# Kernel tuning notes

Hardware: AMD Instinct MI355X
Metric: run time of the kernel (lower is better)

## Reference

```python
import jax, jax.numpy as jnp
import numpy as np
import math

N = 10000; E = 160000; B = 16
H = 256; TD = 128; NB = 4; NL = 3; NAT = 100; CD = 3


def _silu(x):
    return x * jax.nn.sigmoid(x)


def _mlp2(x, w1, b1, w2, b2):
    return _silu(x @ w1 + b1) @ w2 + b2


def _ln(x, g, b):
    m = jnp.mean(x, -1, keepdims=True)
    v = jnp.mean((x - m) ** 2, -1, keepdims=True)
    return (x - m) / jnp.sqrt(v + 1e-5) * g + b


def _fwd(x_atoms, pos, edge_index, batch_idx, timesteps, conditions, emb,
         te_w1, te_b1, te_w2, te_b2, ce_w1, ce_b1, ce_w2, ce_b2,
         tp_w1, tp_b1, tp_w2, tp_b2, nm_w1, nm_b1, nm_w2, nm_b2,
         em_w1, em_b1, em_w2, em_b2, ln_g, ln_b,
         ao_w1, ao_b1, ao_w2, ao_b2, co_w1, co_b1, co_w2, co_b2):
    n = x_atoms.shape[0]
    row, col = edge_index[0], edge_index[1]  # row = source (x_j), col = target (x_i)
    h = emb[x_atoms]  # [N, H]
    half = TD // 2
    freqs = jnp.exp(jnp.arange(half, dtype=jnp.float32) * (-math.log(10000.0) / (half - 1)))
    ang = timesteps.astype(jnp.float32)[:, None] * freqs[None, :]
    time_emb = _mlp2(jnp.concatenate([jnp.sin(ang), jnp.cos(ang)], -1), te_w1, te_b1, te_w2, te_b2)
    time_emb = time_emb + _mlp2(conditions, ce_w1, ce_b1, ce_w2, ce_b2)  # [B, TD]
    rel = pos[row] - pos[col]
    dist = jnp.sqrt(jnp.sum(rel * rel, -1, keepdims=True))  # [E, 1]
    counts = jnp.maximum(
        jax.ops.segment_sum(jnp.ones((row.shape[0],), jnp.float32), col, num_segments=n), 1.0)[:, None]
    for b in range(NB):
        h = h + _mlp2(time_emb, tp_w1[b], tp_b1[b], tp_w2[b], tp_b2[b])[batch_idx]
        for l in range(NL):
            # message: edge_mlp(concat(x_i, x_j, dist)); PyG x_i = target = col, x_j = source = row
            msg = _mlp2(jnp.concatenate([h[col], h[row], dist], -1),
                        em_w1[b, l], em_b1[b, l], em_w2[b, l], em_b2[b, l])  # [E, H]
            agg = jax.ops.segment_sum(msg, col, num_segments=n) / counts  # mean aggregation
            h_new = _mlp2(h, nm_w1[b, l], nm_b1[b, l], nm_w2[b, l], nm_b2[b, l]) + agg
            h = _ln(h + h_new, ln_g[b, l], ln_b[b, l])
    atom = _mlp2(h, ao_w1, ao_b1, ao_w2, ao_b2)  # [N, NAT]
    coord = _mlp2(h, co_w1, co_b1, co_w2, co_b2)  # [N, 3]
    return atom, coord


def setup_inputs() -> dict:
    key = jax.random.key(0)
    ks = jax.random.split(key, 48)
    ki = iter(ks)

    def nrm(shape, s=0.02):
        return jax.random.normal(next(ki), shape, jnp.float32) * s

    x_atoms = jax.random.randint(next(ki), (N,), 0, NAT)
    pos = jax.random.normal(next(ki), (N, 3), jnp.float32)
    row = jax.random.randint(next(ki), (E,), 0, N)
    off = jax.random.randint(next(ki), (E,), 1, N)
    col = (row + off) % N  # avoid self-loops so dist > 0
    edge_index = jnp.stack([row, col])
    batch_idx = jnp.sort(jax.random.randint(next(ki), (N,), 0, B))
    timesteps = jax.random.randint(next(ki), (B,), 0, 1000)
    conditions = jax.random.normal(next(ki), (B, CD), jnp.float32)
    z = lambda s: jnp.zeros(s, jnp.float32)
    params = dict(
        emb=nrm((NAT, H)),
        te_w1=nrm((TD, 2 * TD)), te_b1=z((2 * TD,)), te_w2=nrm((2 * TD, TD)), te_b2=z((TD,)),
        ce_w1=nrm((CD, H)), ce_b1=z((H,)), ce_w2=nrm((H, TD)), ce_b2=z((TD,)),
        tp_w1=nrm((NB, TD, H)), tp_b1=z((NB, H)), tp_w2=nrm((NB, H, H)), tp_b2=z((NB, H)),
        nm_w1=nrm((NB, NL, H, H)), nm_b1=z((NB, NL, H)), nm_w2=nrm((NB, NL, H, H)), nm_b2=z((NB, NL, H)),
        em_w1=nrm((NB, NL, 2 * H + 1, H)), em_b1=z((NB, NL, H)), em_w2=nrm((NB, NL, H, H)), em_b2=z((NB, NL, H)),
        ln_g=jnp.ones((NB, NL, H), jnp.float32), ln_b=z((NB, NL, H)),
        ao_w1=nrm((H, H)), ao_b1=z((H,)), ao_w2=nrm((H, NAT)), ao_b2=z((NAT,)),
        co_w1=nrm((H, H)), co_b1=z((H,)), co_w2=nrm((H, 3)), co_b2=z((3,)),
    )
    return dict(x_atoms=x_atoms, pos=pos, edge_index=edge_index, batch_idx=batch_idx,
                timesteps=timesteps, conditions=conditions, **params)


def reference(x_atoms, pos, edge_index, batch_idx, timesteps, conditions, emb,
              te_w1, te_b1, te_w2, te_b2, ce_w1, ce_b1, ce_w2, ce_b2,
              tp_w1, tp_b1, tp_w2, tp_b2, nm_w1, nm_b1, nm_w2, nm_b2,
              em_w1, em_b1, em_w2, em_b2, ln_g, ln_b,
              ao_w1, ao_b1, ao_w2, ao_b2, co_w1, co_b1, co_w2, co_b2):
    return _fwd(x_atoms, pos, edge_index, batch_idx, timesteps, conditions, emb,
                te_w1, te_b1, te_w2, te_b2, ce_w1, ce_b1, ce_w2, ce_b2,
                tp_w1, tp_b1, tp_w2, tp_b2, nm_w1, nm_b1, nm_w2, nm_b2,
                em_w1, em_b1, em_w2, em_b2, ln_g, ln_b,
                ao_w1, ao_b1, ao_w2, ao_b2, co_w1, co_b1, co_w2, co_b2)
```

## Files before the change

kernel.cpp:

```cpp
#include <hip/hip_runtime.h>

typedef unsigned short u16;
typedef __attribute__((ext_vector_type(8))) short   bf16x8;
typedef __attribute__((ext_vector_type(4))) float   f32x4;
typedef __attribute__((ext_vector_type(4))) unsigned short u16x4;
typedef __attribute__((ext_vector_type(2))) unsigned short u16x2;

#define DEV __device__ __forceinline__

DEV float bf2f(u16 u){ return __uint_as_float(((unsigned)u)<<16); }
DEV u16 f2bf(float f){ unsigned x=__float_as_uint(f); unsigned r=x+0x7fffu+((x>>16)&1u); return (u16)(r>>16); }
DEV float silu_f(float x){
  float e = __expf(-x);
  return x * __builtin_amdgcn_rcpf(1.f + e);
}
DEV float ldf(const void* p, long i, int isbf){
  float r;
  if (isbf) r = bf2f(((const u16*)p)[i]);
  else      r = ((const float*)p)[i];
  return r;
}
template<int ISBF> DEV float LD(const void* p, long i){
  if (ISBF) return bf2f(((const u16*)p)[i]);
  return ((const float*)p)[i];
}

#define GLDS(g,l) __builtin_amdgcn_global_load_lds((const __attribute__((address_space(1))) void*)(g), (__attribute__((address_space(3))) void*)(l), 16, 0, 0)

DEV int xcd_swz(int bid, int nwg){
  int q = nwg >> 3, r = nwg & 7;
  int x = bid & 7, l = bid >> 3;
  return (x < r ? x*(q+1) : r*(q+1) + (x-r)*q) + l;
}

__global__ __launch_bounds__(256) void k_packparams(
    const void* nm_b1, const void* em_b1, const void* nm_b2, const void* em_b2,
    const void* ln_g, const void* ln_b, const void* em_w1,
    const void* ao_b1, const void* co_b1, const void* ao_b2,
    const void* co_w2, const void* co_b2,
    int* __restrict__ flagp, float* __restrict__ pp){
  int isbf = (((const unsigned*)ln_g)[0] == 0x3F800000u) ? 0 : 1;
  int i = blockIdx.x*256 + threadIdx.x;
  if (i == 0) flagp[0] = isbf;
  if (i >= 22887) return;
  const int T1 = 3072;
  float v;
  if      (i < T1)    v = ldf(nm_b1, i, isbf);
  else if (i < 2*T1)  v = ldf(em_b1, i-T1, isbf);
  else if (i < 3*T1)  v = ldf(nm_b2, i-2*T1, isbf);
  else if (i < 4*T1)  v = ldf(em_b2, i-3*T1, isbf);
  else if (i < 5*T1)  v = ldf(ln_g, i-4*T1, isbf);
  else if (i < 6*T1)  v = ldf(ln_b, i-5*T1, isbf);
  else if (i < 7*T1){ int j=i-6*T1; int li=j>>8; v = ldf(em_w1, (long)li*513*256 + 512*256 + (j&255), isbf); }
  else if (i < 22016){ int j=i-21504; v = (j<256) ? ldf(ao_b1,j,isbf) : ldf(co_b1,j-256,isbf); }
  else if (i < 22116) v = ldf(ao_b2, i-22016, isbf);
  else if (i < 22884) v = ldf(co_w2, i-22116, isbf);
  else                v = ldf(co_b2, i-22884, isbf);
  pp[i] = v;
}

struct WTJob {
  const void* in; long inoff; long ims; long obase; long oms;
  u16* out; int istride; int Ncin; int ors; int gx; int gy;
};
struct WTJobs { WTJob j[8]; int tile0[8]; };

template<int ISBF>
DEV void wtall_body(const WTJobs& J){
  int bidx = blockIdx.x;
  int ji = 0;
  #pragma unroll
  for (int j=1;j<8;j++) if (bidx >= J.tile0[j]) ji = j;
  const WTJob& job = J.j[ji];
  int ti = bidx - J.tile0[ji];
  int kx = ti % job.gx;
  int jy = (ti / job.gx) % job.gy;
  long m  = ti / (job.gx * job.gy);
  int k0 = kx*64, j0 = jy*64;
  __shared__ float tile[64][65];
  int t = threadIdx.x;
  int c = t & 63, r4 = t >> 6;
  #pragma unroll
  for (int pass=0; pass<16; pass++){
    int k = k0 + pass*4 + r4;
    int j = j0 + c;
    float v = 0.f;
    if (j < job.Ncin) v = LD<ISBF>(job.in, job.inoff + m*job.ims + (long)k*job.istride + j);
    tile[pass*4 + r4][c] = v;
  }
  __syncthreads();
  #pragma unroll
  for (int pass=0; pass<16; pass++){
    int j = j0 + pass*4 + r4;
    int k = k0 + c;
    job.out[m*job.oms + job.obase + (long)j*job.ors + k] = f2bf(tile[c][pass*4 + r4]);
  }
}
__global__ __launch_bounds__(256) void k_wtall(WTJobs J, const int* __restrict__ flagp){
  if (flagp[0]) wtall_body<1>(J);
  else          wtall_body<0>(J);
}

template<int ISBF>
DEV void time_body(const int* tsteps, const void* cond,
    const void* te_w1, const void* te_b1, const void* te_w2, const void* te_b2,
    const void* ce_w1, const void* ce_b1, const void* ce_w2, const void* ce_b2,
    const void* tp_w1, const void* tp_b1, const void* tp_w2, const void* tp_b2,
    float* tpe){
  __shared__ float wbuf[8192];
  __shared__ float sa[256], sb[256], tm[256], tb[128];
  int b4 = blockIdx.x >> 4, b = blockIdx.x & 15, t = threadIdx.x;
  float ts = (float)tsteps[b];
  if (t < 64){
    float coef = (float)(-9.210340371976184/63.0);
    float fr = __expf(coef * (float)t);
    float ang = ts * fr;
    sa[t]      = sinf(ang);
    sa[64 + t] = cosf(ang);
  }
  __syncthreads();
  float a1 = LD<ISBF>(te_b1, t);
  for (int ck=0; ck<128; ck+=32){
    for (int i=t;i<8192;i+=256) wbuf[i] = LD<ISBF>(te_w1, (long)ck*256 + i);
    __syncthreads();
    #pragma unroll 8
    for (int k=0;k<32;k++) a1 += sa[ck+k]*wbuf[k*256+t];
    __syncthreads();
  }
  sb[t] = silu_f(a1);
  float te = (t<128) ? LD<ISBF>(te_b2, t) : 0.f;
  for (int ck=0; ck<256; ck+=64){
    for (int i=t;i<8192;i+=256) wbuf[i] = LD<ISBF>(te_w2, (long)ck*128 + i);
    __syncthreads();
    if (t<128){
      #pragma unroll 8
      for (int k=0;k<64;k++) te += sb[ck+k]*wbuf[k*128+t];
    }
    __syncthreads();
  }
  float a2 = LD<ISBF>(ce_b1, t);
  #pragma unroll
  for (int k=0;k<3;k++) a2 += LD<ISBF>(cond, b*3+k)*LD<ISBF>(ce_w1, k*256+t);
  sa[t] = silu_f(a2);
  float ce = (t<128) ? LD<ISBF>(ce_b2, t) : 0.f;
  for (int ck=0; ck<256; ck+=64){
    for (int i=t;i<8192;i+=256) wbuf[i] = LD<ISBF>(ce_w2, (long)ck*128 + i);
    __syncthreads();
    if (t<128){
      #pragma unroll 8
      for (int k=0;k<64;k++) ce += sa[ck+k]*wbuf[k*128+t];
    }
    __syncthreads();
  }
  if (t<128) tb[t] = te + ce;
  float a3 = LD<ISBF>(tp_b1, b4*256 + t);
  for (int ck=0; ck<128; ck+=32){
    for (int i=t;i<8192;i+=256) wbuf[i] = LD<ISBF>(tp_w1, ((long)b4*128+ck)*256 + i);
    __syncthreads();
    #pragma unroll 8
    for (int k=0;k<32;k++) a3 += tb[ck+k]*wbuf[k*256+t];
    __syncthreads();
  }
  tm[t] = silu_f(a3);
  float a4 = LD<ISBF>(tp_b2, b4*256 + t);
  for (int ck=0; ck<256; ck+=32){
    for (int i=t;i<8192;i+=256) wbuf[i] = LD<ISBF>(tp_w2, ((long)b4*256+ck)*256 + i);
    __syncthreads();
    #pragma unroll 8
    for (int k=0;k<32;k++) a4 += tm[ck+k]*wbuf[k*256+t];
    __syncthreads();
  }
  tpe[((long)b4*16 + b)*256 + t] = a4;
}
__global__ __launch_bounds__(256) void k_time(
    const int* tsteps, const void* cond,
    const void* te_w1, const void* te_b1, const void* te_w2, const void* te_b2,
    const void* ce_w1, const void* ce_b1, const void* ce_w2, const void* ce_b2,
    const void* tp_w1, const void* tp_b1, const void* tp_w2, const void* tp_b2,
    const int* __restrict__ flagp, float* tpe){
  if (flagp[0]) time_body<1>(tsteps,cond,te_w1,te_b1,te_w2,te_b2,ce_w1,ce_b1,ce_w2,ce_b2,tp_w1,tp_b1,tp_w2,tp_b2,tpe);
  else          time_body<0>(tsteps,cond,te_w1,te_b1,te_w2,te_b2,ce_w1,ce_b1,ce_w2,ce_b2,tp_w1,tp_b1,tp_w2,tp_b2,tpe);
}

template<int ISBF>
DEV void edgegeo_body(const int* ei, const void* pos, float* dist, int* cnt, int E){
  int e = blockIdx.x*256 + threadIdx.x;
  if (e >= E) return;
  int r = ei[e], c = ei[E + e];
  float dx = LD<ISBF>(pos,(long)r*3+0) - LD<ISBF>(pos,(long)c*3+0);
  float dy = LD<ISBF>(pos,(long)r*3+1) - LD<ISBF>(pos,(long)c*3+1);
  float dz = LD<ISBF>(pos,(long)r*3+2) - LD<ISBF>(pos,(long)c*3+2);
  dist[e] = sqrtf(dx*dx + dy*dy + dz*dz);
  atomicAdd(&cnt[c], 1);
}
__global__ __launch_bounds__(256) void k_edgegeo(const int* ei, const void* pos,
                          const int* __restrict__ flagp, float* dist, int* cnt, int E){
  if (flagp[0]) edgegeo_body<1>(ei,pos,dist,cnt,E);
  else          edgegeo_body<0>(ei,pos,dist,cnt,E);
}

__global__ __launch_bounds__(1024) void k_scan(const int* __restrict__ cnt, int* __restrict__ basep, int n){
  __shared__ int wsum[16];
  int t = threadIdx.x, w = t >> 6, lane = t & 63;
  int running = 0;
  int nch = (n + 1023) >> 10;
  for (int ch=0; ch<nch; ch++){
    int i = ch*1024 + t;
    int v = (i < n) ? cnt[i] : 0;
    int sc = v;
    #pragma unroll
    for (int off=1; off<64; off<<=1){
      int u = __shfl_up(sc, off, 64);
      if (lane >= off) sc += u;
    }
    if (lane == 63) wsum[w] = sc;
    __syncthreads();
    int wexcl = 0, tot = 0;
    #pragma unroll
    for (int j=0;j<16;j++){ int x = wsum[j]; if (j < w) wexcl += x; tot += x; }
    if (i < n) basep[i] = running + wexcl + sc - v;
    running += tot;
    __syncthreads();
  }
  if (t == 0) basep[n] = running;
}

__global__ __launch_bounds__(256) void k_scatter(const int* __restrict__ ei, const int* __restrict__ basep,
                          int* __restrict__ cursor, int* __restrict__ perm, int E){
  int e = blockIdx.x*256 + threadIdx.x;
  if (e >= E) return;
  int c = ei[E + e];
  int p = atomicAdd(&cursor[c], 1);
  perm[basep[c] + p] = e;
}

template<int ISBF>
DEV void embed_body(const int* xa, const void* emb, const float* tpe0, const int* bidx,
                    float* h, u16* hb, int total){
  int idx = blockIdx.x*256 + threadIdx.x;
  if (idx >= total) return;
  int row = idx >> 8, col = idx & 255;
  float v = LD<ISBF>(emb, (long)xa[row]*256 + col) + tpe0[bidx[row]*256 + col];
  h[idx] = v;
  hb[idx] = f2bf(v);
}
__global__ __launch_bounds__(256) void k_embed(const int* xa, const void* emb,
                        const int* __restrict__ flagp, const float* tpe0, const int* bidx,
                        float* h, u16* hb, int total){
  if (flagp[0]) embed_body<1>(xa, emb, tpe0, bidx, h, hb, total);
  else          embed_body<0>(xa, emb, tpe0, bidx, h, hb, total);
}

__global__ __launch_bounds__(256) void k_agg(
    const u16* __restrict__ PQ, const int* __restrict__ perm, const int* __restrict__ basep,
    const int* __restrict__ rows, const float* __restrict__ dist,
    const float* __restrict__ w1rf, const float* __restrict__ b1f,
    const int* __restrict__ cnt, u16* __restrict__ A2, int n){
  int w = threadIdx.x >> 6, lane = threadIdx.x & 63;
  int node = blockIdx.x*2 + (w >> 1);
  if (node >= n) return;
  int half = w & 1;
  int c0 = half*128 + lane*2;
  u16x2 pv = *(const u16x2*)&PQ[(long)node*512 + c0];
  float pb0 = bf2f(pv[0]) + b1f[c0];
  float pb1 = bf2f(pv[1]) + b1f[c0+1];
  float wr0 = w1rf[c0], wr1 = w1rf[c0+1];
  float acc0 = 0.f, acc1 = 0.f;
  int s = basep[node], e = basep[node+1];
  const u16* Qb = PQ + 256 + c0;
  for (int q0=s; q0<e; q0+=64){
    int m = e - q0; if (m > 64) m = 64;
    int   rl = 0; float dl = 0.f;
    if (lane < m){ int ed = perm[q0+lane]; rl = rows[ed]; dl = dist[ed]; }
    int q = 0;
    for (; q+4<=m; q+=4){
      int   r0 = __shfl(rl, q,   64), r1 = __shfl(rl, q+1, 64);
      int   r2 = __shfl(rl, q+2, 64), r3 = __shfl(rl, q+3, 64);
      float d0 = __shfl(dl, q,   64), d1 = __shfl(dl, q+1, 64);
      float d2 = __shfl(dl, q+2, 64), d3 = __shfl(dl, q+3, 64);
      u16x2 qv0 = *(const u16x2*)&Qb[(long)r0*512];
      u16x2 qv1 = *(const u16x2*)&Qb[(long)r1*512];
      u16x2 qv2 = *(const u16x2*)&Qb[(long)r2*512];
      u16x2 qv3 = *(const u16x2*)&Qb[(long)r3*512];
      acc0 += silu_f(fmaf(d0, wr0, pb0 + bf2f(qv0[0])));
      acc1 += silu_f(fmaf(d0, wr1, pb1 + bf2f(qv0[1])));
      acc0 += silu_f(fmaf(d1, wr0, pb0 + bf2f(qv1[0])));
      acc1 += silu_f(fmaf(d1, wr1, pb1 + bf2f(qv1[1])));
      acc0 += silu_f(fmaf(d2, wr0, pb0 + bf2f(qv2[0])));
      acc1 += silu_f(fmaf(d2, wr1, pb1 + bf2f(qv2[1])));
      acc0 += silu_f(fmaf(d3, wr0, pb0 + bf2f(qv3[0])));
      acc1 += silu_f(fmaf(d3, wr1, pb1 + bf2f(qv3[1])));
    }
    for (; q<m; q++){
      int   r = __shfl(rl, q, 64);
      float d = __shfl(dl, q, 64);
      u16x2 qv = *(const u16x2*)&Qb[(long)r*512];
      acc0 += silu_f(fmaf(d, wr0, pb0 + bf2f(qv[0])));
      acc1 += silu_f(fmaf(d, wr1, pb1 + bf2f(qv[1])));
    }
  }
  int cc = cnt[node];
  float inv = __builtin_amdgcn_rcpf((float)(cc > 0 ? cc : 1));
  u16x2 o; o[0] = f2bf(acc0*inv); o[1] = f2bf(acc1*inv);
  *(u16x2*)&A2[(long)node*512 + 256 + c0] = o;
}

__global__ __launch_bounds__(256) void k_co2(
    const u16* __restrict__ UV, const float* __restrict__ w, const float* __restrict__ b,
    const int* __restrict__ flagp, void* __restrict__ out, long n100, int n){
  int isbf = flagp[0];
  int row = blockIdx.x*4 + (threadIdx.x >> 6);
  if (row >= n) return;
  int lane = threadIdx.x & 63;
  int k0 = lane*4;
  u16x4 vv = *(const u16x4*)&UV[(long)row*512 + 256 + k0];
  float a0=0.f, a1=0.f, a2=0.f;
  #pragma unroll
  for (int j=0;j<4;j++){
    float v = bf2f(vv[j]);
    a0 += v*w[(k0+j)*3+0];
    a1 += v*w[(k0+j)*3+1];
    a2 += v*w[(k0+j)*3+2];
  }
  #pragma unroll
  for (int o=32;o>=1;o>>=1){ a0 += __shfl_xor(a0,o,64); a1 += __shfl_xor(a1,o,64); a2 += __shfl_xor(a2,o,64); }
  if (lane == 0){
    float r0 = a0 + b[0], r1 = a1 + b[1], r2 = a2 + b[2];
    if (isbf){
      u16* o = (u16*)out + n100 + (long)row*3;
      o[0] = f2bf(r0); o[1] = f2bf(r1); o[2] = f2bf(r2);
    } else {
      float* o = (float*)out + n100 + (long)row*3;
      o[0] = r0; o[1] = r1; o[2] = r2;
    }
  }
}

template<int TM, int MODE>
__global__ __launch_bounds__(256) void k_gemm(
    const u16* __restrict__ A, int lda, const u16* __restrict__ Wt,
    void* __restrict__ D0, void* __restrict__ D1,
    const float* __restrict__ bf1,
    const int* __restrict__ flagp, int M, int K, int nbn){
  constexpr int MR = TM/32;
  __shared__ __align__(16) u16 As[TM*64];
  __shared__ __align__(16) u16 Bs[128*64];
  const int bid = xcd_swz(blockIdx.x, gridDim.x);
  const int mb = bid / nbn, nb = bid - mb*nbn;
  const int bm0 = mb*TM, bn0 = nb*128;
  const int t = threadIdx.x;
  const int w = t >> 6, lane = t & 63;
  const int wr = w >> 1, wc = w & 1;
  const int swz8 = ((lane & 7) ^ (lane >> 3)) * 8;

  f32x4 acc[MR][4];
  #pragma unroll
  for (int m=0;m<MR;m++)
    #pragma unroll
    for (int n=0;n<4;n++){ f32x4 z = {0.f,0.f,0.f,0.f}; acc[m][n] = z; }

  long baseA[TM/32];
  #pragma unroll
  for (int i=0;i<TM/32;i++){
    int r = bm0 + i*32 + w*8 + (lane>>3);
    if (r > M-1) r = M-1;
    baseA[i] = (long)r*lda + swz8;
  }
  long baseB[4];
  #pragma unroll
  for (int i=0;i<4;i++){
    int r = bn0 + i*32 + w*8 + (lane>>3);
    baseB[i] = (long)r*K + swz8;
  }

  const int rA = lane & 15;
  const int sx = rA & 7;
  const int qhi = lane >> 4;

  for (int kt=0; kt<K; kt+=64){
    #pragma unroll
    for (int i=0;i<TM/32;i++) GLDS(A  + baseA[i] + kt, As + (i*32 + w*8)*64);
    #pragma unroll
    for (int i=0;i<4;i++)     GLDS(Wt + baseB[i] + kt, Bs + (i*32 + w*8)*64);
    __syncthreads();
    #pragma unroll
    for (int kk=0;kk<2;kk++){
      const int punit = ((kk*4 + qhi) ^ sx) * 8;
      bf16x8 af[MR], bv[4];
      #pragma unroll
      for (int m=0;m<MR;m++)
        af[m] = *(const bf16x8*)&As[(wr*(TM/2) + m*16 + rA)*64 + punit];
      #pragma unroll
      for (int n=0;n<4;n++)
        bv[n] = *(const bf16x8*)&Bs[(wc*64 + n*16 + rA)*64 + punit];
      #pragma unroll
      for (int m=0;m<MR;m++)
        #pragma unroll
        for (int n=0;n<4;n++)
          acc[m][n] = __builtin_amdgcn_mfma_f32_16x16x32_bf16(af[m], bv[n], acc[m][n], 0, 0, 0);
    }
    __syncthreads();
  }

  const int rg = lane >> 4, cix = lane & 15;
  const int isbf = (MODE==3) ? flagp[0] : 0;
  #pragma unroll
  for (int n=0;n<4;n++){
    const int col = bn0 + wc*64 + n*16 + cix;
    float b1v = 0.f;
    if (MODE==0){ if (col>=512) b1v = bf1[col-512]; }
    else if (MODE==2){ b1v = bf1[col]; }
    else { if (col<100) b1v = bf1[col]; }
    #pragma unroll
    for (int m=0;m<MR;m++){
      const int rbase = bm0 + wr*(TM/2) + m*16 + rg*4;
      #pragma unroll
      for (int r=0;r<4;r++){
        const int row = rbase + r;
        if (row >= M) continue;
        float v = acc[m][n][r];
        if (MODE==0){
          if (col < 512) ((u16*)D0)[(long)row*512 + col] = f2bf(v);
          else           ((u16*)D1)[(long)row*512 + (col-512)] = f2bf(silu_f(v + b1v));
        } else if (MODE==2){
          ((u16*)D0)[(long)row*512 + col] = f2bf(silu_f(v + b1v));
        } else {
          if (col < 100){
            v += b1v;
            if (isbf) ((u16*)D0)[(long)row*100 + col] = f2bf(v);
            else      ((float*)D0)[(long)row*100 + col] = v;
          }
        }
      }
    }
  }
}

__global__ __launch_bounds__(256) void k_gemmln(
    const u16* __restrict__ A, const u16* __restrict__ Wt,
    float* __restrict__ h, u16* __restrict__ hb,
    const float* __restrict__ b1f, const float* __restrict__ b2f,
    const float* __restrict__ gf, const float* __restrict__ bbf,
    const int* __restrict__ cnt,
    const float* __restrict__ tpe, const int* __restrict__ bidx,
    int M, int K){
  __shared__ __align__(16) u16 As[32*64];
  __shared__ __align__(16) u16 Bs[256*64];
  const int bm0 = blockIdx.x*32;
  const int t = threadIdx.x;
  const int w = t >> 6, lane = t & 63;
  const int wc = w;
  const int swz8 = ((lane & 7) ^ (lane >> 3)) * 8;

  f32x4 acc[2][4];
  #pragma unroll
  for (int m=0;m<2;m++)
    #pragma unroll
    for (int n=0;n<4;n++){ f32x4 z = {0.f,0.f,0.f,0.f}; acc[m][n] = z; }

  long baseA;
  { int r = bm0 + w*8 + (lane>>3); if (r > M-1) r = M-1; baseA = (long)r*512 + swz8; }
  long baseB[8];
  #pragma unroll
  for (int i=0;i<8;i++){
    int r = i*32 + w*8 + (lane>>3);
    baseB[i] = (long)r*K + swz8;
  }

  const int rA = lane & 15;
  const int sx = rA & 7;
  const int qhi = lane >> 4;

  for (int kt=0; kt<K; kt+=64){
    GLDS(A + baseA + kt, As + (w*8)*64);
    #pragma unroll
    for (int i=0;i<8;i++) GLDS(Wt + baseB[i] + kt, Bs + (i*32 + w*8)*64);
    __syncthreads();
    #pragma unroll
    for (int kk=0;kk<2;kk++){
      const int punit = ((kk*4 + qhi) ^ sx) * 8;
      bf16x8 af[2], bv[4];
      #pragma unroll
      for (int m=0;m<2;m++)
        af[m] = *(const bf16x8*)&As[(m*16 + rA)*64 + punit];
      #pragma unroll
      for (int n=0;n<4;n++)
        bv[n] = *(const bf16x8*)&Bs[(wc*64 + n*16 + rA)*64 + punit];
      #pragma unroll
      for (int m=0;m<2;m++)
        #pragma unroll
        for (int n=0;n<4;n++)
          acc[m][n] = __builtin_amdgcn_mfma_f32_16x16x32_bf16(af[m], bv[n], acc[m][n], 0, 0, 0);
    }
    __syncthreads();
  }

  const int rg = lane >> 4, cix = lane & 15;
  float ps[2][4], pq[2][4];
  #pragma unroll
  for (int m=0;m<2;m++){
    #pragma unroll
    for (int r=0;r<4;r++){
      const int row = bm0 + m*16 + rg*4 + r;
      const int rowc = (row < M) ? row : (M-1);
      const float hmask = (cnt[rowc] > 0) ? 1.f : 0.f;
      float s = 0.f, q = 0.f;
      #pragma unroll
      for (int n=0;n<4;n++){
        const int col = wc*64 + n*16 + cix;
        float v = acc[m][n][r] + b1f[col] + hmask*b2f[col] + h[(long)rowc*256 + col];
        acc[m][n][r] = v;
        s += v; q += v*v;
      }
      ps[m][r] = s; pq[m][r] = q;
    }
  }
  #pragma unroll
  for (int m=0;m<2;m++)
    #pragma unroll
    for (int r=0;r<4;r++){
      #pragma unroll
      for (int o=8;o>=1;o>>=1){
        ps[m][r] += __shfl_xor(ps[m][r], o, 64);
        pq[m][r] += __shfl_xor(pq[m][r], o, 64);
      }
    }
  float* sred = (float*)As;
  if (cix == 0){
    #pragma unroll
    for (int m=0;m<2;m++)
      #pragma unroll
      for (int r=0;r<4;r++){
        int rl = m*16 + rg*4 + r;
        sred[w*32 + rl]       = ps[m][r];
        sred[128 + w*32 + rl] = pq[m][r];
      }
  }
  __syncthreads();
  #pragma unroll
  for (int m=0;m<2;m++){
    #pragma unroll
    for (int r=0;r<4;r++){
      const int rl = m*16 + rg*4 + r;
      const int row = bm0 + rl;
      if (row >= M) continue;
      float S = sred[rl] + sred[32+rl] + sred[64+rl] + sred[96+rl];
      float Q = sred[128+rl] + sred[160+rl] + sred[192+rl] + sred[224+rl];
      float mean = S * (1.f/256.f);
      float var  = Q * (1.f/256.f) - mean*mean;
      float rs = rsqrtf(var + 1e-5f);
      const float* tb = tpe ? (tpe + (long)bidx[row]*256) : nullptr;
      #pragma unroll
      for (int n=0;n<4;n++){
        const int col = wc*64 + n*16 + cix;
        float y = (acc[m][n][r]-mean)*rs*gf[col] + bbf[col];
        if (tb) y += tb[col];
        h[(long)row*256 + col] = y;
        hb[(long)row*256 + col] = f2bf(y);
      }
    }
  }
}

extern "C" void kernel_launch(void* const* d_in, const int* in_sizes, int n_in,
                              void* d_out, int out_size, void* d_ws, size_t ws_size,
                              hipStream_t stream)
{
  const int N  = in_sizes[0];
  const int E  = in_sizes[2] / 2;
  const int H  = 256;
  const int MB128 = (N + 127)/128;
  const int MB64  = (N + 63)/64;
  const int MB32  = (N + 31)/32;

  const int*  x_atoms = (const int*)d_in[0];
  const void* pos     = d_in[1];
  const int*  ei      = (const int*)d_in[2];
  const int*  bidx    = (const int*)d_in[3];
  const int*  tsteps  = (const int*)d_in[4];
  const void* cond    = d_in[5];
  const void* emb     = d_in[6];
  const void* te_w1   = d_in[7];
  const void* te_b1   = d_in[8];
  const void* te_w2   = d_in[9];
  const void* te_b2   = d_in[10];
  const void* ce_w1   = d_in[11];
  const void* ce_b1   = d_in[12];
  const void* ce_w2   = d_in[13];
  const void* ce_b2   = d_in[14];
  const void* tp_w1   = d_in[15];
  const void* tp_b1   = d_in[16];
  const void* tp_w2   = d_in[17];
  const void* tp_b2   = d_in[18];
  const void* nm_w1   = d_in[19];
  const void* nm_b1   = d_in[20];
  const void* nm_w2   = d_in[21];
  const void* nm_b2   = d_in[22];
  const void* em_w1   = d_in[23];
  const void* em_b1   = d_in[24];
  const void* em_w2   = d_in[25];
  const void* em_b2   = d_in[26];
  const void* ln_g    = d_in[27];
  const void* ln_b    = d_in[28];
  const void* ao_w1   = d_in[29];
  const void* ao_b1   = d_in[30];
  const void* ao_w2   = d_in[31];
  const void* ao_b2   = d_in[32];
  const void* co_w1   = d_in[33];
  const void* co_b1   = d_in[34];
  const void* co_w2   = d_in[35];
  const void* co_b2   = d_in[36];

  char* wp = (char*)d_ws;
  auto alloc = [&](size_t bytes)->char*{ char* p = wp; wp += (bytes + 255) & ~(size_t)255; return p; };
  int*   flagp   = (int*)  alloc(256);
  float* h_f32   = (float*)alloc((size_t)N*H*4);
  u16*   hb16    = (u16*)  alloc((size_t)N*H*2);
  u16*   PQ      = (u16*)  alloc((size_t)N*512*2);
  u16*   A2      = (u16*)  alloc((size_t)N*512*2);
  u16*   UV      = PQ;
  float* dist    = (float*)alloc((size_t)E*4);
  int*   perm    = (int*)  alloc((size_t)E*4);
  int*   basep   = (int*)  alloc((size_t)(N+1)*4);
  int*   cnt     = (int*)  alloc((size_t)N*4);
  int*   cursor  = (int*)  alloc((size_t)N*4);
  float* tpe     = (float*)alloc((size_t)4*16*256*4);
  u16*   pqtW    = (u16*)  alloc((size_t)12*768*256*2);
  u16*   w2stk   = (u16*)  alloc((size_t)12*256*512*2);
  u16*   UVw     = (u16*)  alloc((size_t)512*256*2);
  u16*   ao_w2t  = (u16*)  alloc((size_t)128*256*2);
  float* pp      = (float*)alloc((size_t)22887*4);

  const float* nm_b1f = pp;
  const float* em_b1f = pp + 3072;
  const float* nm_b2f = pp + 6144;
  const float* em_b2f = pp + 9216;
  const float* ln_gf  = pp + 12288;
  const float* ln_bf  = pp + 15360;
  const float* w1rf   = pp + 18432;
  const float* headbf = pp + 21504;
  const float* ao_b2f = pp + 22016;
  const float* co_w2f = pp + 22116;
  const float* co_b2f = pp + 22884;

  hipMemsetAsync(cnt,    0, (size_t)N*4, stream);
  hipMemsetAsync(cursor, 0, (size_t)N*4, stream);

  k_packparams<<<(22887+255)/256, 256, 0, stream>>>(nm_b1, em_b1, nm_b2, em_b2, ln_g, ln_b, em_w1,
                                                    ao_b1, co_b1, ao_b2, co_w2, co_b2, flagp, pp);

  WTJobs J;
  auto setjob = [&](int idx, const void* in, long inoff, long ims, int istride, int Ncin,
                    u16* out, long obase, int ors, long oms, int gx, int gy, int gz){
    J.j[idx] = WTJob{ in, inoff, ims, obase, oms, out, istride, Ncin, ors, gx, gy };
    J.tile0[idx] = (idx == 0) ? 0 : 0;
    return gx*gy*gz;
  };
  int tacc = 0;
  int tn;
  tn = setjob(0, em_w1, 0,        513*256, 256, 256, pqtW,  0,        256, 768*256, 4, 4, 12); J.tile0[0]=tacc; tacc+=tn;
  tn = setjob(1, em_w1, 256*256,  513*256, 256, 256, pqtW,  256*256,  256, 768*256, 4, 4, 12); J.tile0[1]=tacc; tacc+=tn;
  tn = setjob(2, nm_w1, 0,        256*256, 256, 256, pqtW,  512*256,  256, 768*256, 4, 4, 12); J.tile0[2]=tacc; tacc+=tn;
  tn = setjob(3, nm_w2, 0,        256*256, 256, 256, w2stk, 0,        512, 256*512, 4, 4, 12); J.tile0[3]=tacc; tacc+=tn;
  tn = setjob(4, em_w2, 0,        256*256, 256, 256, w2stk, 256,      512, 256*512, 4, 4, 12); J.tile0[4]=tacc; tacc+=tn;
  tn = setjob(5, ao_w1, 0,        0,       256, 256, UVw,   0,        256, 0,       4, 4, 1);  J.tile0[5]=tacc; tacc+=tn;
  tn = setjob(6, co_w1, 0,        0,       256, 256, UVw,   256*256,  256, 0,       4, 4, 1);  J.tile0[6]=tacc; tacc+=tn;
  tn = setjob(7, ao_w2, 0,        0,       100, 100, ao_w2t,0,        256, 0,       4, 2, 1);  J.tile0[7]=tacc; tacc+=tn;
  k_wtall<<<tacc, 256, 0, stream>>>(J, flagp);

  k_time<<<64, 256, 0, stream>>>(tsteps, cond, te_w1, te_b1, te_w2, te_b2,
                                 ce_w1, ce_b1, ce_w2, ce_b2,
                                 tp_w1, tp_b1, tp_w2, tp_b2, flagp, tpe);

  k_edgegeo<<<(E+255)/256, 256, 0, stream>>>(ei, pos, flagp, dist, cnt, E);
  k_scan<<<1, 1024, 0, stream>>>(cnt, basep, N);
  k_scatter<<<(E+255)/256, 256, 0, stream>>>(ei, basep, cursor, perm, E);

  k_embed<<<(N*H+255)/256, 256, 0, stream>>>(x_atoms, emb, flagp, tpe, bidx, h_f32, hb16, N*H);

  for (int b4 = 0; b4 < 4; b4++){
    for (int l = 0; l < 3; l++){
      int li = b4*3 + l;
      k_gemm<128,0><<<MB128*6, 256, 0, stream>>>(hb16, 256, pqtW + (long)li*768*256,
                                                 PQ, A2, nm_b1f + li*256,
                                                 flagp, N, 256, 6);
      k_agg<<<(N+1)/2, 256, 0, stream>>>(PQ, perm, basep, ei, dist,
                                         w1rf + li*256, em_b1f + li*256, cnt, A2, N);
      const float* tpe_next = (l == 2 && b4 < 3) ? (tpe + (long)(b4+1)*16*256) : nullptr;
      k_gemmln<<<MB32, 256, 0, stream>>>(A2, w2stk + (long)li*256*512,
                                         h_f32, hb16,
                                         nm_b2f + li*256, em_b2f + li*256,
                                         ln_gf + li*256, ln_bf + li*256,
                                         cnt, tpe_next, bidx, N, 512);
    }
  }

  k_gemm<128,2><<<MB128*4, 256, 0, stream>>>(hb16, 256, UVw, UV, nullptr, headbf,
                                             flagp, N, 256, 4);
  k_gemm<64,3><<<MB64*1, 256, 0, stream>>>(UV, 512, ao_w2t, d_out, nullptr, ao_b2f,
                                           flagp, N, 256, 1);
  k_co2<<<(N+3)/4, 256, 0, stream>>>(UV, co_w2f, co_b2f, flagp, d_out, (long)N*100, N);
}
```

Measured before the change: 875.2 us.

## Fuse startup kernels and merge edge aggregation into LayerNorm GEMM

Four preprocessing launches (time MLP, weight transposes, param packing, edge geometry) are merged into one k_startup kernel, with the f32 time path double-buffered through global_load_lds. Scatter and embed are fused into one launch, and the dtype flag is now taken from ln_g inside each kernel instead of from a device flag. Per-layer k_agg and k_gemmln are merged into k_aggln, which aggregates edges into LDS and feeds that directly into the second GEMM. This drops the A2 intermediate buffer and several launches, but the fused kernel does more work per block and runs on fewer blocks (MB32).

```diff
diff --git a/kernel.cpp b/kernel.cpp
--- a/kernel.cpp
+++ b/kernel.cpp
@@ -24,6 +24,9 @@
   if (ISBF) return bf2f(((const u16*)p)[i]);
   return ((const float*)p)[i];
 }
+DEV int detect_bf(const void* lng){
+  return (((const unsigned*)lng)[0] == 0x3F800000u) ? 0 : 1;
+}
 
 #define GLDS(g,l) __builtin_amdgcn_global_load_lds((const __attribute__((address_space(1))) void*)(g), (__attribute__((address_space(3))) void*)(l), 16, 0, 0)
 
@@ -33,15 +36,48 @@
   return (x < r ? x*(q+1) : r*(q+1) + (x-r)*q) + l;
 }
 
-__global__ __launch_bounds__(256) void k_packparams(
+struct WTJob {
+  const void* in; u16* out;
+  int inoff, ims, obase, oms, istride, Ncin, ors, gx, gy;
+};
+struct WTJobs { WTJob j[8]; int tile0[8]; };
+
+template<int ISBF>
+DEV void wtall_body(const WTJobs& J, int bidx, float* tile ){
+  int ji = 0;
+  #pragma unroll
+  for (int j=1;j<8;j++) if (bidx >= J.tile0[j]) ji = j;
+  const WTJob& job = J.j[ji];
+  int ti = bidx - J.tile0[ji];
+  int kx = ti % job.gx;
+  int jy = (ti / job.gx) % job.gy;
+  long m  = ti / (job.gx * job.gy);
+  int k0 = kx*64, j0 = jy*64;
+  int t = threadIdx.x;
+  int c = t & 63, r4 = t >> 6;
+  #pragma unroll
+  for (int pass=0; pass<16; pass++){
+    int k = k0 + pass*4 + r4;
+    int j = j0 + c;
+    float v = 0.f;
+    if (j < job.Ncin) v = LD<ISBF>(job.in, (long)job.inoff + m*job.ims + (long)k*job.istride + j);
+    tile[(pass*4 + r4)*65 + c] = v;
+  }
+  __syncthreads();
+  #pragma unroll
+  for (int pass=0; pass<16; pass++){
+    int j = j0 + pass*4 + r4;
+    int k = k0 + c;
+    job.out[m*job.oms + job.obase + (long)j*job.ors + k] = f2bf(tile[c*65 + pass*4 + r4]);
+  }
+}
+
+DEV void pack_body(int pb, int isbf,
     const void* nm_b1, const void* em_b1, const void* nm_b2, const void* em_b2,
     const void* ln_g, const void* ln_b, const void* em_w1,
     const void* ao_b1, const void* co_b1, const void* ao_b2,
-    const void* co_w2, const void* co_b2,
-    int* __restrict__ flagp, float* __restrict__ pp){
-  int isbf = (((const unsigned*)ln_g)[0] == 0x3F800000u) ? 0 : 1;
-  int i = blockIdx.x*256 + threadIdx.x;
-  if (i == 0) flagp[0] = isbf;
+    const void* co_w2, const void* co_b2, float* pp){
+  int i = pb*256 + threadIdx.x;
   if (i >= 22887) return;
   const int T1 = 3072;
   float v;
@@ -59,132 +95,9 @@
   pp[i] = v;
 }
 
-struct WTJob {
-  const void* in; long inoff; long ims; long obase; long oms;
-  u16* out; int istride; int Ncin; int ors; int gx; int gy;
-};
-struct WTJobs { WTJob j[8]; int tile0[8]; };
-
 template<int ISBF>
-DEV void wtall_body(const WTJobs& J){
-  int bidx = blockIdx.x;
-  int ji = 0;
-  #pragma unroll
-  for (int j=1;j<8;j++) if (bidx >= J.tile0[j]) ji = j;
-  const WTJob& job = J.j[ji];
-  int ti = bidx - J.tile0[ji];
-  int kx = ti % job.gx;
-  int jy = (ti / job.gx) % job.gy;
-  long m  = ti / (job.gx * job.gy);
-  int k0 = kx*64, j0 = jy*64;
-  __shared__ float tile[64][65];
-  int t = threadIdx.x;
-  int c = t & 63, r4 = t >> 6;
-  #pragma unroll
-  for (int pass=0; pass<16; pass++){
-    int k = k0 + pass*4 + r4;
-    int j = j0 + c;
-    float v = 0.f;
-    if (j < job.Ncin) v = LD<ISBF>(job.in, job.inoff + m*job.ims + (long)k*job.istride + j);
-    tile[pass*4 + r4][c] = v;
-  }
-  __syncthreads();
-  #pragma unroll
-  for (int pass=0; pass<16; pass++){
-    int j = j0 + pass*4 + r4;
-    int k = k0 + c;
-    job.out[m*job.oms + job.obase + (long)j*job.ors + k] = f2bf(tile[c][pass*4 + r4]);
-  }
-}
-__global__ __launch_bounds__(256) void k_wtall(WTJobs J, const int* __restrict__ flagp){
-  if (flagp[0]) wtall_body<1>(J);
-  else          wtall_body<0>(J);
-}
-
-template<int ISBF>
-DEV void time_body(const int* tsteps, const void* cond,
-    const void* te_w1, const void* te_b1, const void* te_w2, const void* te_b2,
-    const void* ce_w1, const void* ce_b1, const void* ce_w2, const void* ce_b2,
-    const void* tp_w1, const void* tp_b1, const void* tp_w2, const void* tp_b2,
-    float* tpe){
-  __shared__ float wbuf[8192];
-  __shared__ float sa[256], sb[256], tm[256], tb[128];
-  int b4 = blockIdx.x >> 4, b = blockIdx.x & 15, t = threadIdx.x;
-  float ts = (float)tsteps[b];
-  if (t < 64){
-    float coef = (float)(-9.210340371976184/63.0);
-    float fr = __expf(coef * (float)t);
-    float ang = ts * fr;
-    sa[t]      = sinf(ang);
-    sa[64 + t] = cosf(ang);
-  }
-  __syncthreads();
-  float a1 = LD<ISBF>(te_b1, t);
-  for (int ck=0; ck<128; ck+=32){
-    for (int i=t;i<8192;i+=256) wbuf[i] = LD<ISBF>(te_w1, (long)ck*256 + i);
-    __syncthreads();
-    #pragma unroll 8
-    for (int k=0;k<32;k++) a1 += sa[ck+k]*wbuf[k*256+t];
-    __syncthreads();
-  }
-  sb[t] = silu_f(a1);
-  float te = (t<128) ? LD<ISBF>(te_b2, t) : 0.f;
-  for (int ck=0; ck<256; ck+=64){
-    for (int i=t;i<8192;i+=256) wbuf[i] = LD<ISBF>(te_w2, (long)ck*128 + i);
-    __syncthreads();
-    if (t<128){
-      #pragma unroll 8
-      for (int k=0;k<64;k++) te += sb[ck+k]*wbuf[k*128+t];
-    }
-    __syncthreads();
-  }
-  float a2 = LD<ISBF>(ce_b1, t);
-  #pragma unroll
-  for (int k=0;k<3;k++) a2 += LD<ISBF>(cond, b*3+k)*LD<ISBF>(ce_w1, k*256+t);
-  sa[t] = silu_f(a2);
-  float ce = (t<128) ? LD<ISBF>(ce_b2, t) : 0.f;
-  for (int ck=0; ck<256; ck+=64){
-    for (int i=t;i<8192;i+=256) wbuf[i] = LD<ISBF>(ce_w2, (long)ck*128 + i);
-    __syncthreads();
-    if (t<128){
-      #pragma unroll 8
-      for (int k=0;k<64;k++) ce += sa[ck+k]*wbuf[k*128+t];
-    }
-    __syncthreads();
-  }
-  if (t<128) tb[t] = te + ce;
-  float a3 = LD<ISBF>(tp_b1, b4*256 + t);
-  for (int ck=0; ck<128; ck+=32){
-    for (int i=t;i<8192;i+=256) wbuf[i] = LD<ISBF>(tp_w1, ((long)b4*128+ck)*256 + i);
-    __syncthreads();
-    #pragma unroll 8
-    for (int k=0;k<32;k++) a3 += tb[ck+k]*wbuf[k*256+t];
-    __syncthreads();
-  }
-  tm[t] = silu_f(a3);
-  float a4 = LD<ISBF>(tp_b2, b4*256 + t);
-  for (int ck=0; ck<256; ck+=32){
-    for (int i=t;i<8192;i+=256) wbuf[i] = LD<ISBF>(tp_w2, ((long)b4*256+ck)*256 + i);
-    __syncthreads();
-    #pragma unroll 8
-    for (int k=0;k<32;k++) a4 += tm[ck+k]*wbuf[k*256+t];
-    __syncthreads();
-  }
-  tpe[((long)b4*16 + b)*256 + t] = a4;
-}
-__global__ __launch_bounds__(256) void k_time(
-    const int* tsteps, const void* cond,
-    const void* te_w1, const void* te_b1, const void* te_w2, const void* te_b2,
-    const void* ce_w1, const void* ce_b1, const void* ce_w2, const void* ce_b2,
-    const void* tp_w1, const void* tp_b1, const void* tp_w2, const void* tp_b2,
-    const int* __restrict__ flagp, float* tpe){
-  if (flagp[0]) time_body<1>(tsteps,cond,te_w1,te_b1,te_w2,te_b2,ce_w1,ce_b1,ce_w2,ce_b2,tp_w1,tp_b1,tp_w2,tp_b2,tpe);
-  else          time_body<0>(tsteps,cond,te_w1,te_b1,te_w2,te_b2,ce_w1,ce_b1,ce_w2,ce_b2,tp_w1,tp_b1,tp_w2,tp_b2,tpe);
-}
-
-template<int ISBF>
-DEV void edgegeo_body(const int* ei, const void* pos, float* dist, int* cnt, int E){
-  int e = blockIdx.x*256 + threadIdx.x;
+DEV void edgegeo_body(int eb, const int* ei, const void* pos, float* dist, int* cnt, int E){
+  int e = eb*256 + threadIdx.x;
   if (e >= E) return;
   int r = ei[e], c = ei[E + e];
   float dx = LD<ISBF>(pos,(long)r*3+0) - LD<ISBF>(pos,(long)c*3+0);
@@ -193,10 +106,185 @@
   dist[e] = sqrtf(dx*dx + dy*dy + dz*dz);
   atomicAdd(&cnt[c], 1);
 }
-__global__ __launch_bounds__(256) void k_edgegeo(const int* ei, const void* pos,
-                          const int* __restrict__ flagp, float* dist, int* cnt, int E){
-  if (flagp[0]) edgegeo_body<1>(ei,pos,dist,cnt,E);
-  else          edgegeo_body<0>(ei,pos,dist,cnt,E);
+
+DEV void time_body_f32(const int* tsteps, const float* cond,
+    const float* te_w1,const float* te_b1,const float* te_w2,const float* te_b2,
+    const float* ce_w1,const float* ce_b1,const float* ce_w2,const float* ce_b2,
+    const float* tp_w1,const float* tp_b1,const float* tp_w2,const float* tp_b2,
+    float* tpe, float* smem){
+  float* wbuf = smem;
+  float* sa = smem + 16384;
+  float* sb = sa + 256;
+  float* tm = sb + 256;
+  float* tb = tm + 256;
+  const int b4 = blockIdx.x >> 4, b = blockIdx.x & 15, t = threadIdx.x;
+  const int wbase = (t >> 6) * 256;
+
+  auto TISSUE = [&](const float* src, int buf){
+    float* d = wbuf + buf*8192 + wbase;
+    #pragma unroll
+    for (int r=0;r<8;r++)
+      GLDS(src + (long)r*1024 + t*4, d + r*1024);
+  };
+
+  float ts = (float)tsteps[b];
+  if (t < 64){
+    float coef = (float)(-9.210340371976184/63.0);
+    float fr = __expf(coef * (float)t);
+    float ang = ts * fr;
+    sa[t] = sinf(ang); sa[64+t] = cosf(ang);
+  }
+  TISSUE(te_w1, 0);
+  __syncthreads();
+  float a1 = te_b1[t];
+  for (int c=0;c<4;c++){
+    if (c<3) TISSUE(te_w1 + (c+1)*8192, (c+1)&1);
+    const float* wb = wbuf + (c&1)*8192;
+    #pragma unroll 8
+    for (int k=0;k<32;k++) a1 = fmaf(sa[c*32+k], wb[k*256+t], a1);
+    __syncthreads();
+  }
+  sb[t] = silu_f(a1);
+  TISSUE(te_w2, 0);
+  __syncthreads();
+  float te = (t<128) ? te_b2[t] : 0.f;
+  for (int c=0;c<4;c++){
+    if (c<3) TISSUE(te_w2 + (c+1)*8192, (c+1)&1);
+    const float* wb = wbuf + (c&1)*8192;
+    if (t < 128){
+      #pragma unroll 8
+      for (int k=0;k<64;k++) te = fmaf(sb[c*64+k], wb[k*128+t], te);
+    }
+    __syncthreads();
+  }
+  {
+    float a2 = ce_b1[t];
+    #pragma unroll
+    for (int k=0;k<3;k++) a2 = fmaf(cond[b*3+k], ce_w1[k*256+t], a2);
+    sa[t] = silu_f(a2);
+  }
+  TISSUE(ce_w2, 0);
+  __syncthreads();
+  float ce = (t<128) ? ce_b2[t] : 0.f;
+  for (int c=0;c<4;c++){
+    if (c<3) TISSUE(ce_w2 + (c+1)*8192, (c+1)&1);
+    const float* wb = wbuf + (c&1)*8192;
+    if (t < 128){
+      #pragma unroll 8
+      for (int k=0;k<64;k++) ce = fmaf(sa[c*64+k], wb[k*128+t], ce);
+    }
+    __syncthreads();
+  }
+  if (t < 128) tb[t] = te + ce;
+  const float* W5 = tp_w1 + (long)b4*128*256;
+  TISSUE(W5, 0);
+  __syncthreads();
+  float a3 = tp_b1[b4*256 + t];
+  for (int c=0;c<4;c++){
+    if (c<3) TISSUE(W5 + (c+1)*8192, (c+1)&1);
+    const float* wb = wbuf + (c&1)*8192;
+    #pragma unroll 8
+    for (int k=0;k<32;k++) a3 = fmaf(tb[c*32+k], wb[k*256+t], a3);
+    __syncthreads();
+  }
+  tm[t] = silu_f(a3);
+  const float* W6 = tp_w2 + (long)b4*256*256;
+  TISSUE(W6, 0);
+  __syncthreads();
+  float a4 = tp_b2[b4*256 + t];
+  for (int c=0;c<8;c++){
+    if (c<7) TISSUE(W6 + (c+1)*8192, (c+1)&1);
+    const float* wb = wbuf + (c&1)*8192;
+    #pragma unroll 8
+    for (int k=0;k<32;k++) a4 = fmaf(tm[c*32+k], wb[k*256+t], a4);
+    __syncthreads();
+  }
+  tpe[((long)b4*16 + b)*256 + t] = a4;
+}
+
+DEV void time_body_bf16(const int* tsteps, const u16* cond,
+    const u16* te_w1,const u16* te_b1,const u16* te_w2,const u16* te_b2,
+    const u16* ce_w1,const u16* ce_b1,const u16* ce_w2,const u16* ce_b2,
+    const u16* tp_w1,const u16* tp_b1,const u16* tp_w2,const u16* tp_b2,
+    float* tpe, float* smem){
+  float* sa = smem; float* sb = smem+256; float* tm = smem+512; float* tb = smem+768;
+  int b4 = blockIdx.x >> 4, b = blockIdx.x & 15, t = threadIdx.x;
+  float ts = (float)tsteps[b];
+  if (t < 64){
+    float coef = (float)(-9.210340371976184/63.0);
+    float fr = __expf(coef * (float)t);
+    float ang = ts * fr;
+    sa[t] = sinf(ang); sa[64+t] = cosf(ang);
+  }
+  __syncthreads();
+  float a1 = bf2f(te_b1[t]);
+  for (int k=0;k<128;k++) a1 += sa[k]*bf2f(te_w1[k*256+t]);
+  __syncthreads();
+  sb[t] = silu_f(a1);
+  __syncthreads();
+  float te = 0.f;
+  if (t<128){
+    te = bf2f(te_b2[t]);
+    for (int k=0;k<256;k++) te += sb[k]*bf2f(te_w2[k*128+t]);
+  }
+  float a2 = bf2f(ce_b1[t]);
+  for (int k=0;k<3;k++) a2 += bf2f(cond[b*3+k])*bf2f(ce_w1[k*256+t]);
+  float t2v = silu_f(a2);
+  __syncthreads();
+  sa[t] = t2v;
+  __syncthreads();
+  if (t<128){
+    float ce = bf2f(ce_b2[t]);
+    for (int k=0;k<256;k++) ce += sa[k]*bf2f(ce_w2[k*128+t]);
+    tb[t] = te + ce;
+  }
+  __syncthreads();
+  float a3 = bf2f(tp_b1[b4*256+t]);
+  for (int k=0;k<128;k++) a3 += tb[k]*bf2f(tp_w1[((long)b4*128+k)*256+t]);
+  __syncthreads();
+  tm[t] = silu_f(a3);
+  __syncthreads();
+  float a4 = bf2f(tp_b2[b4*256+t]);
+  for (int k=0;k<256;k++) a4 += tm[k]*bf2f(tp_w2[((long)b4*256+k)*256+t]);
+  tpe[((long)b4*16+b)*256+t] = a4;
+}
+
+__global__ __launch_bounds__(256) void k_startup(
+    const int* tsteps, const void* cond,
+    const void* te_w1,const void* te_b1,const void* te_w2,const void* te_b2,
+    const void* ce_w1,const void* ce_b1,const void* ce_w2,const void* ce_b2,
+    const void* tp_w1,const void* tp_b1,const void* tp_w2,const void* tp_b2,
+    float* tpe,
+    WTJobs J, int wt_n,
+    const void* nm_b1,const void* em_b1,const void* nm_b2,const void* em_b2,
+    const void* ln_g,const void* ln_b,const void* em_w1,
+    const void* ao_b1,const void* co_b1,const void* ao_b2,const void* co_w2,const void* co_b2,
+    float* pp, int pack_n,
+    const int* ei, const void* pos, float* dist, int* cnt, int E)
+{
+  __shared__ __align__(16) float smem[17408];
+  const int isbf = detect_bf(ln_g);
+  int b = blockIdx.x;
+  if (b < 64){
+    if (isbf) time_body_bf16(tsteps, (const u16*)cond,
+        (const u16*)te_w1,(const u16*)te_b1,(const u16*)te_w2,(const u16*)te_b2,
+        (const u16*)ce_w1,(const u16*)ce_b1,(const u16*)ce_w2,(const u16*)ce_b2,
+        (const u16*)tp_w1,(const u16*)tp_b1,(const u16*)tp_w2,(const u16*)tp_b2, tpe, smem);
+    else time_body_f32(tsteps, (const float*)cond,
+        (const float*)te_w1,(const float*)te_b1,(const float*)te_w2,(const float*)te_b2,
+        (const float*)ce_w1,(const float*)ce_b1,(const float*)ce_w2,(const float*)ce_b2,
+        (const float*)tp_w1,(const float*)tp_b1,(const float*)tp_w2,(const float*)tp_b2, tpe, smem);
+  } else if (b < 64 + wt_n){
+    if (isbf) wtall_body<1>(J, b-64, smem);
+    else      wtall_body<0>(J, b-64, smem);
+  } else if (b < 64 + wt_n + pack_n){
+    pack_body(b - 64 - wt_n, isbf, nm_b1, em_b1, nm_b2, em_b2, ln_g, ln_b, em_w1,
+              ao_b1, co_b1, ao_b2, co_w2, co_b2, pp);
+  } else {
+    int eb = b - 64 - wt_n - pack_n;
+    if (isbf) edgegeo_body<1>(eb, ei, pos, dist, cnt, E);
+    else      edgegeo_body<0>(eb, ei, pos, dist, cnt, E);
+  }
 }
 
 __global__ __launch_bounds__(1024) void k_scan(const int* __restrict__ cnt, int* __restrict__ basep, int n){
@@ -225,90 +313,35 @@
   if (t == 0) basep[n] = running;
 }
 
-__global__ __launch_bounds__(256) void k_scatter(const int* __restrict__ ei, const int* __restrict__ basep,
-                          int* __restrict__ cursor, int* __restrict__ perm, int E){
-  int e = blockIdx.x*256 + threadIdx.x;
-  if (e >= E) return;
-  int c = ei[E + e];
-  int p = atomicAdd(&cursor[c], 1);
-  perm[basep[c] + p] = e;
-}
-
-template<int ISBF>
-DEV void embed_body(const int* xa, const void* emb, const float* tpe0, const int* bidx,
-                    float* h, u16* hb, int total){
-  int idx = blockIdx.x*256 + threadIdx.x;
-  if (idx >= total) return;
-  int row = idx >> 8, col = idx & 255;
-  float v = LD<ISBF>(emb, (long)xa[row]*256 + col) + tpe0[bidx[row]*256 + col];
-  h[idx] = v;
-  hb[idx] = f2bf(v);
-}
-__global__ __launch_bounds__(256) void k_embed(const int* xa, const void* emb,
-                        const int* __restrict__ flagp, const float* tpe0, const int* bidx,
-                        float* h, u16* hb, int total){
-  if (flagp[0]) embed_body<1>(xa, emb, tpe0, bidx, h, hb, total);
-  else          embed_body<0>(xa, emb, tpe0, bidx, h, hb, total);
-}
-
-__global__ __launch_bounds__(256) void k_agg(
-    const u16* __restrict__ PQ, const int* __restrict__ perm, const int* __restrict__ basep,
-    const int* __restrict__ rows, const float* __restrict__ dist,
-    const float* __restrict__ w1rf, const float* __restrict__ b1f,
-    const int* __restrict__ cnt, u16* __restrict__ A2, int n){
-  int w = threadIdx.x >> 6, lane = threadIdx.x & 63;
-  int node = blockIdx.x*2 + (w >> 1);
-  if (node >= n) return;
-  int half = w & 1;
-  int c0 = half*128 + lane*2;
-  u16x2 pv = *(const u16x2*)&PQ[(long)node*512 + c0];
-  float pb0 = bf2f(pv[0]) + b1f[c0];
-  float pb1 = bf2f(pv[1]) + b1f[c0+1];
-  float wr0 = w1rf[c0], wr1 = w1rf[c0+1];
-  float acc0 = 0.f, acc1 = 0.f;
-  int s = basep[node], e = basep[node+1];
-  const u16* Qb = PQ + 256 + c0;
-  for (int q0=s; q0<e; q0+=64){
-    int m = e - q0; if (m > 64) m = 64;
-    int   rl = 0; float dl = 0.f;
-    if (lane < m){ int ed = perm[q0+lane]; rl = rows[ed]; dl = dist[ed]; }
-    int q = 0;
-    for (; q+4<=m; q+=4){
-      int   r0 = __shfl(rl, q,   64), r1 = __shfl(rl, q+1, 64);
-      int   r2 = __shfl(rl, q+2, 64), r3 = __shfl(rl, q+3, 64);
-      float d0 = __shfl(dl, q,   64), d1 = __shfl(dl, q+1, 64);
-      float d2 = __shfl(dl, q+2, 64), d3 = __shfl(dl, q+3, 64);
-      u16x2 qv0 = *(const u16x2*)&Qb[(long)r0*512];
-      u16x2 qv1 = *(const u16x2*)&Qb[(long)r1*512];
-      u16x2 qv2 = *(const u16x2*)&Qb[(long)r2*512];
-      u16x2 qv3 = *(const u16x2*)&Qb[(long)r3*512];
-      acc0 += silu_f(fmaf(d0, wr0, pb0 + bf2f(qv0[0])));
-      acc1 += silu_f(fmaf(d0, wr1, pb1 + bf2f(qv0[1])));
-      acc0 += silu_f(fmaf(d1, wr0, pb0 + bf2f(qv1[0])));
-      acc1 += silu_f(fmaf(d1, wr1, pb1 + bf2f(qv1[1])));
-      acc0 += silu_f(fmaf(d2, wr0, pb0 + bf2f(qv2[0])));
-      acc1 += silu_f(fmaf(d2, wr1, pb1 + bf2f(qv2[1])));
-      acc0 += silu_f(fmaf(d3, wr0, pb0 + bf2f(qv3[0])));
-      acc1 += silu_f(fmaf(d3, wr1, pb1 + bf2f(qv3[1])));
-    }
-    for (; q<m; q++){
-      int   r = __shfl(rl, q, 64);
-      float d = __shfl(dl, q, 64);
-      u16x2 qv = *(const u16x2*)&Qb[(long)r*512];
-      acc0 += silu_f(fmaf(d, wr0, pb0 + bf2f(qv[0])));
-      acc1 += silu_f(fmaf(d, wr1, pb1 + bf2f(qv[1])));
-    }
-  }
-  int cc = cnt[node];
-  float inv = __builtin_amdgcn_rcpf((float)(cc > 0 ? cc : 1));
-  u16x2 o; o[0] = f2bf(acc0*inv); o[1] = f2bf(acc1*inv);
-  *(u16x2*)&A2[(long)node*512 + 256 + c0] = o;
+__global__ __launch_bounds__(256) void k_scatter_embed(
+    const int* __restrict__ ei, const int* __restrict__ basep,
+    int* __restrict__ cursor, int* __restrict__ perm, int E,
+    const int* __restrict__ xa, const void* __restrict__ emb, const void* __restrict__ lng,
+    const float* __restrict__ tpe0, const int* __restrict__ bidx,
+    float* __restrict__ h, u16* __restrict__ hb, int totalh){
+  int b = blockIdx.x, t = threadIdx.x;
+  int nsb = (E + 255) >> 8;
+  if (b < nsb){
+    int e = b*256 + t;
+    if (e >= E) return;
+    int c = ei[E + e];
+    int p = atomicAdd(&cursor[c], 1);
+    perm[basep[c] + p] = e;
+  } else {
+    int isbf = detect_bf(lng);
+    int idx = (b - nsb)*256 + t;
+    if (idx >= totalh) return;
+    int row = idx >> 8, col = idx & 255;
+    float v = ldf(emb, (long)xa[row]*256 + col, isbf) + tpe0[bidx[row]*256 + col];
+    h[idx] = v;
+    hb[idx] = f2bf(v);
+  }
 }
 
 __global__ __launch_bounds__(256) void k_co2(
     const u16* __restrict__ UV, const float* __restrict__ w, const float* __restrict__ b,
-    const int* __restrict__ flagp, void* __restrict__ out, long n100, int n){
-  int isbf = flagp[0];
+    const void* __restrict__ lng, void* __restrict__ out, long n100, int n){
+  int isbf = detect_bf(lng);
   int row = blockIdx.x*4 + (threadIdx.x >> 6);
   if (row >= n) return;
   int lane = threadIdx.x & 63;
@@ -341,7 +374,7 @@
     const u16* __restrict__ A, int lda, const u16* __restrict__ Wt,
     void* __restrict__ D0, void* __restrict__ D1,
     const float* __restrict__ bf1,
-    const int* __restrict__ flagp, int M, int K, int nbn){
+    const void* __restrict__ lng, int M, int K, int nbn){
   constexpr int MR = TM/32;
   __shared__ __align__(16) u16 As[TM*64];
   __shared__ __align__(16) u16 Bs[128*64];
@@ -403,7 +436,7 @@
   }
 
   const int rg = lane >> 4, cix = lane & 15;
-  const int isbf = (MODE==3) ? flagp[0] : 0;
+  const int isbf = (MODE==3) ? detect_bf(lng) : 0;
   #pragma unroll
   for (int n=0;n<4;n++){
     const int col = bn0 + wc*64 + n*16 + cix;
@@ -421,7 +454,7 @@
         float v = acc[m][n][r];
         if (MODE==0){
           if (col < 512) ((u16*)D0)[(long)row*512 + col] = f2bf(v);
-          else           ((u16*)D1)[(long)row*512 + (col-512)] = f2bf(silu_f(v + b1v));
+          else           ((u16*)D1)[(long)row*256 + (col-512)] = f2bf(silu_f(v + b1v));
         } else if (MODE==2){
           ((u16*)D0)[(long)row*512 + col] = f2bf(silu_f(v + b1v));
         } else {
@@ -436,53 +469,127 @@
   }
 }
 
-__global__ __launch_bounds__(256) void k_gemmln(
-    const u16* __restrict__ A, const u16* __restrict__ Wt,
+__global__ __launch_bounds__(256) void k_aggln(
+    const u16* __restrict__ Tb, const u16* __restrict__ PQ, const u16* __restrict__ Wt,
     float* __restrict__ h, u16* __restrict__ hb,
+    const int* __restrict__ perm, const int* __restrict__ basep,
+    const int* __restrict__ rows, const float* __restrict__ dist,
+    const float* __restrict__ w1rf, const float* __restrict__ em_b1f,
     const float* __restrict__ b1f, const float* __restrict__ b2f,
     const float* __restrict__ gf, const float* __restrict__ bbf,
     const int* __restrict__ cnt,
     const float* __restrict__ tpe, const int* __restrict__ bidx,
-    int M, int K){
+    int M){
+  __shared__ __align__(16) u16 SnB[32*256];
   __shared__ __align__(16) u16 As[32*64];
   __shared__ __align__(16) u16 Bs[256*64];
   const int bm0 = blockIdx.x*32;
   const int t = threadIdx.x;
   const int w = t >> 6, lane = t & 63;
-  const int wc = w;
   const int swz8 = ((lane & 7) ^ (lane >> 3)) * 8;
 
-  f32x4 acc[2][4];
-  #pragma unroll
-  for (int m=0;m<2;m++)
-    #pragma unroll
-    for (int n=0;n<4;n++){ f32x4 z = {0.f,0.f,0.f,0.f}; acc[m][n] = z; }
-
   long baseA;
-  { int r = bm0 + w*8 + (lane>>3); if (r > M-1) r = M-1; baseA = (long)r*512 + swz8; }
+  { int r = bm0 + w*8 + (lane>>3); if (r > M-1) r = M-1; baseA = (long)r*256 + swz8; }
   long baseB[8];
   #pragma unroll
   for (int i=0;i<8;i++){
     int r = i*32 + w*8 + (lane>>3);
-    baseB[i] = (long)r*K + swz8;
-  }
+    baseB[i] = (long)r*512 + swz8;
+  }
+  GLDS(Tb + baseA, As + (w*8)*64);
+  #pragma unroll
+  for (int i=0;i<8;i++) GLDS(Wt + baseB[i], Bs + (i*32 + w*8)*64);
+
+  {
+    const int c0 = lane*4;
+    float wr_[4], eb[4];
+    #pragma unroll
+    for (int k2=0;k2<4;k2++){ wr_[k2] = w1rf[c0+k2]; eb[k2] = em_b1f[c0+k2]; }
+    const int bqu = lane >> 4;
+    const int ui  = (lane >> 1) & 7;
+    const int e4  = (lane & 1) * 4;
+    for (int j=0;j<8;j++){
+      const int node = bm0 + w*8 + j;
+      const int rl = w*8 + j;
+      u16x4 o = {0,0,0,0};
+      if (node < M){
+        u16x4 pv = *(const u16x4*)&PQ[(long)node*512 + c0];
+        float pb[4];
+        #pragma unroll
+        for (int k2=0;k2<4;k2++) pb[k2] = bf2f(pv[k2]) + eb[k2];
+        float acc4[4] = {0.f,0.f,0.f,0.f};
+        int s = basep[node], e = basep[node+1];
+        const u16* Qb = PQ + 256 + c0;
+        for (int q0=s; q0<e; q0+=64){
+          int m = e - q0; if (m > 64) m = 64;
+          int rl2 = 0; float dl = 0.f;
+          if (lane < m){ int ed = perm[q0+lane]; rl2 = rows[ed]; dl = dist[ed]; }
+          int q = 0;
+          for (; q+4<=m; q+=4){
+            int   r0 = __shfl(rl2, q,   64), r1 = __shfl(rl2, q+1, 64);
+            int   r2 = __shfl(rl2, q+2, 64), r3 = __shfl(rl2, q+3, 64);
+            float d0 = __shfl(dl,  q,   64), d1 = __shfl(dl,  q+1, 64);
+            float d2 = __shfl(dl,  q+2, 64), d3 = __shfl(dl,  q+3, 64);
+            u16x4 qv0 = *(const u16x4*)&Qb[(long)r0*512];
+            u16x4 qv1 = *(const u16x4*)&Qb[(long)r1*512];
+            u16x4 qv2 = *(const u16x4*)&Qb[(long)r2*512];
+            u16x4 qv3 = *(const u16x4*)&Qb[(long)r3*512];
+            #pragma unroll
+            for (int k2=0;k2<4;k2++){
+              acc4[k2] += silu_f(fmaf(d0, wr_[k2], pb[k2] + bf2f(qv0[k2])));
+              acc4[k2] += silu_f(fmaf(d1, wr_[k2], pb[k2] + bf2f(qv1[k2])));
+              acc4[k2] += silu_f(fmaf(d2, wr_[k2], pb[k2] + bf2f(qv2[k2])));
+              acc4[k2] += silu_f(fmaf(d3, wr_[k2], pb[k2] + bf2f(qv3[k2])));
+            }
+          }
+          for (; q<m; q++){
+            int   r = __shfl(rl2, q, 64);
+            float d = __shfl(dl,  q, 64);
+            u16x4 qv = *(const u16x4*)&Qb[(long)r*512];
+            #pragma unroll
+            for (int k2=0;k2<4;k2++)
+              acc4[k2] += silu_f(fmaf(d, wr_[k2], pb[k2] + bf2f(qv[k2])));
+          }
+        }
+        int cc = cnt[node];
+        float inv = __builtin_amdgcn_rcpf((float)(cc > 0 ? cc : 1));
+        #pragma unroll
+        for (int k2=0;k2<4;k2++) o[k2] = f2bf(acc4[k2]*inv);
+      }
+      *(u16x4*)&SnB[rl*256 + bqu*64 + ((ui ^ j) << 3) + e4] = o;
+    }
+  }
+  __syncthreads();
+
+  const int wc = w;
+  f32x4 acc[2][4];
+  #pragma unroll
+  for (int m=0;m<2;m++)
+    #pragma unroll
+    for (int n=0;n<4;n++){ f32x4 z = {0.f,0.f,0.f,0.f}; acc[m][n] = z; }
 
   const int rA = lane & 15;
   const int sx = rA & 7;
   const int qhi = lane >> 4;
 
-  for (int kt=0; kt<K; kt+=64){
-    GLDS(A + baseA + kt, As + (w*8)*64);
-    #pragma unroll
-    for (int i=0;i<8;i++) GLDS(Wt + baseB[i] + kt, Bs + (i*32 + w*8)*64);
-    __syncthreads();
+  for (int kt=0; kt<512; kt+=64){
+    if (kt > 0){
+      if (kt < 256) GLDS(Tb + baseA + kt, As + (w*8)*64);
+      #pragma unroll
+      for (int i=0;i<8;i++) GLDS(Wt + baseB[i] + kt, Bs + (i*32 + w*8)*64);
+      __syncthreads();
+    }
     #pragma unroll
     for (int kk=0;kk<2;kk++){
       const int punit = ((kk*4 + qhi) ^ sx) * 8;
       bf16x8 af[2], bv[4];
-      #pragma unroll
-      for (int m=0;m<2;m++)
-        af[m] = *(const bf16x8*)&As[(m*16 + rA)*64 + punit];
+      if (kt < 256){
+        #pragma unroll
+        for (int m=0;m<2;m++) af[m] = *(const bf16x8*)&As[(m*16 + rA)*64 + punit];
+      } else {
+        #pragma unroll
+        for (int m=0;m<2;m++) af[m] = *(const bf16x8*)&SnB[(m*16 + rA)*256 + (kt - 256) + punit];
+      }
       #pragma unroll
       for (int n=0;n<4;n++)
         bv[n] = *(const bf16x8*)&Bs[(wc*64 + n*16 + rA)*64 + punit];
@@ -613,17 +720,17 @@
 
   char* wp = (char*)d_ws;
   auto alloc = [&](size_t bytes)->char*{ char* p = wp; wp += (bytes + 255) & ~(size_t)255; return p; };
-  int*   flagp   = (int*)  alloc(256);
   float* h_f32   = (float*)alloc((size_t)N*H*4);
   u16*   hb16    = (u16*)  alloc((size_t)N*H*2);
   u16*   PQ      = (u16*)  alloc((size_t)N*512*2);
-  u16*   A2      = (u16*)  alloc((size_t)N*512*2);
+  u16*   Tb      = (u16*)  alloc((size_t)N*256*2);
   u16*   UV      = PQ;
   float* dist    = (float*)alloc((size_t)E*4);
   int*   perm    = (int*)  alloc((size_t)E*4);
   int*   basep   = (int*)  alloc((size_t)(N+1)*4);
-  int*   cnt     = (int*)  alloc((size_t)N*4);
-  int*   cursor  = (int*)  alloc((size_t)N*4);
+  size_t cntpad  = ((size_t)N*4 + 255) & ~(size_t)255;
+  int*   cnt     = (int*)  alloc(2*cntpad);
+  int*   cursor  = (int*)((char*)cnt + cntpad);
   float* tpe     = (float*)alloc((size_t)4*16*256*4);
   u16*   pqtW    = (u16*)  alloc((size_t)12*768*256*2);
   u16*   w2stk   = (u16*)  alloc((size_t)12*256*512*2);
@@ -643,61 +750,60 @@
   const float* co_w2f = pp + 22116;
   const float* co_b2f = pp + 22884;
 
-  hipMemsetAsync(cnt,    0, (size_t)N*4, stream);
-  hipMemsetAsync(cursor, 0, (size_t)N*4, stream);
-
-  k_packparams<<<(22887+255)/256, 256, 0, stream>>>(nm_b1, em_b1, nm_b2, em_b2, ln_g, ln_b, em_w1,
-                                                    ao_b1, co_b1, ao_b2, co_w2, co_b2, flagp, pp);
+  hipMemsetAsync(cnt, 0, 2*cntpad, stream);
 
   WTJobs J;
-  auto setjob = [&](int idx, const void* in, long inoff, long ims, int istride, int Ncin,
-                    u16* out, long obase, int ors, long oms, int gx, int gy, int gz){
-    J.j[idx] = WTJob{ in, inoff, ims, obase, oms, out, istride, Ncin, ors, gx, gy };
-    J.tile0[idx] = (idx == 0) ? 0 : 0;
-    return gx*gy*gz;
+  int tacc = 0;
+  auto setjob = [&](int idx, const void* in, int inoff, int ims, int istride, int Ncin,
+                    u16* out, int obase, int ors, int oms, int gx, int gy, int gz){
+    J.j[idx] = WTJob{ in, out, inoff, ims, obase, oms, istride, Ncin, ors, gx, gy };
+    J.tile0[idx] = tacc;
+    tacc += gx*gy*gz;
   };
-  int tacc = 0;
-  int tn;
-  tn = setjob(0, em_w1, 0,        513*256, 256, 256, pqtW,  0,        256, 768*256, 4, 4, 12); J.tile0[0]=tacc; tacc+=tn;
-  tn = setjob(1, em_w1, 256*256,  513*256, 256, 256, pqtW,  256*256,  256, 768*256, 4, 4, 12); J.tile0[1]=tacc; tacc+=tn;
-  tn = setjob(2, nm_w1, 0,        256*256, 256, 256, pqtW,  512*256,  256, 768*256, 4, 4, 12); J.tile0[2]=tacc; tacc+=tn;
-  tn = setjob(3, nm_w2, 0,        256*256, 256, 256, w2stk, 0,        512, 256*512, 4, 4, 12); J.tile0[3]=tacc; tacc+=tn;
-  tn = setjob(4, em_w2, 0,        256*256, 256, 256, w2stk, 256,      512, 256*512, 4, 4, 12); J.tile0[4]=tacc; tacc+=tn;
-  tn = setjob(5, ao_w1, 0,        0,       256, 256, UVw,   0,        256, 0,       4, 4, 1);  J.tile0[5]=tacc; tacc+=tn;
-  tn = setjob(6, co_w1, 0,        0,       256, 256, UVw,   256*256,  256, 0,       4, 4, 1);  J.tile0[6]=tacc; tacc+=tn;
-  tn = setjob(7, ao_w2, 0,        0,       100, 100, ao_w2t,0,        256, 0,       4, 2, 1);  J.tile0[7]=tacc; tacc+=tn;
-  k_wtall<<<tacc, 256, 0, stream>>>(J, flagp);
-
-  k_time<<<64, 256, 0, stream>>>(tsteps, cond, te_w1, te_b1, te_w2, te_b2,
-                                 ce_w1, ce_b1, ce_w2, ce_b2,
-                                 tp_w1, tp_b1, tp_w2, tp_b2, flagp, tpe);
-
-  k_edgegeo<<<(E+255)/256, 256, 0, stream>>>(ei, pos, flagp, dist, cnt, E);
+  setjob(0, em_w1, 0,        513*256, 256, 256, pqtW,  0,        256, 768*256, 4, 4, 12);
+  setjob(1, em_w1, 256*256,  513*256, 256, 256, pqtW,  256*256,  256, 768*256, 4, 4, 12);
+  setjob(2, nm_w1, 0,        256*256, 256, 256, pqtW,  512*256,  256, 768*256, 4, 4, 12);
+  setjob(3, nm_w2, 0,        256*256, 256, 256, w2stk, 0,        512, 256*512, 4, 4, 12);
+  setjob(4, em_w2, 0,        256*256, 256, 256, w2stk, 256,      512, 256*512, 4, 4, 12);
+  setjob(5, ao_w1, 0,        0,       256, 256, UVw,   0,        256, 0,       4, 4, 1);
+  setjob(6, co_w1, 0,        0,       256, 256, UVw,   256*256,  256, 0,       4, 4, 1);
+  setjob(7, ao_w2, 0,        0,       100, 100, ao_w2t,0,        256, 0,       4, 2, 1);
+  const int wt_n = tacc;
+  const int pack_n = (22887 + 255)/256;
+  const int eg_n = (E + 255)/256;
+  k_startup<<<64 + wt_n + pack_n + eg_n, 256, 0, stream>>>(
+      tsteps, cond, te_w1, te_b1, te_w2, te_b2, ce_w1, ce_b1, ce_w2, ce_b2,
+      tp_w1, tp_b1, tp_w2, tp_b2, tpe,
+      J, wt_n,
+      nm_b1, em_b1, nm_b2, em_b2, ln_g, ln_b, em_w1,
+      ao_b1, co_b1, ao_b2, co_w2, co_b2, pp, pack_n,
+      ei, pos, dist, cnt, E);
+
   k_scan<<<1, 1024, 0, stream>>>(cnt, basep, N);
-  k_scatter<<<(E+255)/256, 256, 0, stream>>>(ei, basep, cursor, perm, E);
-
-  k_embed<<<(N*H+255)/256, 256, 0, stream>>>(x_atoms, emb, flagp, tpe, bidx, h_f32, hb16, N*H);
+
+  k_scatter_embed<<<eg_n + (N*H + 255)/256, 256, 0, stream>>>(
+      ei, basep, cursor, perm, E,
+      x_atoms, emb, ln_g, tpe, bidx, h_f32, hb16, N*H);
 
   for (int b4 = 0; b4 < 4; b4++){
     for (int l = 0; l < 3; l++){
       int li = b4*3 + l;
       k_gemm<128,0><<<MB128*6, 256, 0, stream>>>(hb16, 256, pqtW + (long)li*768*256,
-                                                 PQ, A2, nm_b1f + li*256,
-                                                 flagp, N, 256, 6);
-      k_agg<<<(N+1)/2, 256, 0, stream>>>(PQ, perm, basep, ei, dist,
-                                         w1rf + li*256, em_b1f + li*256, cnt, A2, N);
+                                                 PQ, Tb, nm_b1f + li*256,
+                                                 ln_g, N, 256, 6);
       const float* tpe_next = (l == 2 && b4 < 3) ? (tpe + (long)(b4+1)*16*256) : nullptr;
-      k_gemmln<<<MB32, 256, 0, stream>>>(A2, w2stk + (long)li*256*512,
-                                         h_f32, hb16,
-                                         nm_b2f + li*256, em_b2f + li*256,
-                                         ln_gf + li*256, ln_bf + li*256,
-                                         cnt, tpe_next, bidx, N, 512);
+      k_aggln<<<MB32, 256, 0, stream>>>(Tb, PQ, w2stk + (long)li*256*512,
+                                        h_f32, hb16, perm, basep, ei, dist,
+                                        w1rf + li*256, em_b1f + li*256,
+                                        nm_b2f + li*256, em_b2f + li*256,
+                                        ln_gf + li*256, ln_bf + li*256,
+                                        cnt, tpe_next, bidx, N);
     }
   }
 
   k_gemm<128,2><<<MB128*4, 256, 0, stream>>>(hb16, 256, UVw, UV, nullptr, headbf,
-                                             flagp, N, 256, 4);
+                                             ln_g, N, 256, 4);
   k_gemm<64,3><<<MB64*1, 256, 0, stream>>>(UV, 512, ao_w2t, d_out, nullptr, ao_b2f,
-                                           flagp, N, 256, 1);
-  k_co2<<<(N+3)/4, 256, 0, stream>>>(UV, co_w2f, co_b2f, flagp, d_out, (long)N*100, N);
-}
+                                           ln_g, N, 256, 1);
+  k_co2<<<(N+3)/4, 256, 0, stream>>>(UV, co_w2f, co_b2f, ln_g, d_out, (long)N*100, N);
+}
```

New measurement: 1.045 ms. 1.19x slower.
